# Kernel optimization log

Measured on AMD Instinct MI355X. Metric: run time of the kernel, lower is better.

Reference implementation:

```python
import jax, jax.numpy as jnp
import numpy as np

B, T, H = 4, 512, 512          # batch, num_target_nodes, hidden
V = 32000                       # static vocab
S, SDV = 512, 300               # source nodes, source dynamic vocab
TDV = 512                       # target dynamic vocab


def setup_inputs() -> dict:
    key = jax.random.key(0)
    ks = jax.random.split(key, 9)
    src_idx = jax.random.randint(ks[6], (B, S), 0, SDV)
    tgt_idx = jax.random.randint(ks[8], (B, T), 0, TDV)
    return {
        "hiddens": jax.random.normal(ks[0], (B, T, H), jnp.float32),
        "Wp": jax.random.normal(ks[1], (H, 3), jnp.float32) * (1.0 / np.sqrt(H)),
        "bp": jnp.zeros((3,), jnp.float32),
        "Wv": jax.random.normal(ks[2], (H, V), jnp.float32) * (1.0 / np.sqrt(H)),
        "bv": jnp.zeros((V,), jnp.float32),
        "source_attentions": jax.nn.softmax(jax.random.normal(ks[3], (B, T, S), jnp.float32), axis=-1),
        "source_attention_maps": jax.nn.one_hot(src_idx, SDV, dtype=jnp.float32),
        "target_attentions": jax.nn.softmax(jax.random.normal(ks[4], (B, T, TDV), jnp.float32), axis=-1),
        "target_attention_maps": jax.nn.one_hot(tgt_idx, TDV, dtype=jnp.float32),
    }


def reference(hiddens, Wp, bp, Wv, bv, source_attentions, source_attention_maps,
              target_attentions, target_attention_maps):
    b, t, h = hiddens.shape
    hf = hiddens.reshape(b * t, h)
    # switch probabilities: [copy_source, copy_target, generate]
    p = jax.nn.softmax(hf @ Wp + bp, axis=1).reshape(b, t, 3)
    p_copy_source = p[..., 0:1]
    p_copy_target = p[..., 1:2]
    p_generate = p[..., 2:3]
    # vocab scores with pad index masked to -inf (vocab_pad_idx = 0)
    scores = hf @ Wv + bv                      # [b*t, V]
    scores = scores.at[:, 0].set(-jnp.inf)
    vocab_probs = jax.nn.softmax(scores.reshape(b, t, -1), axis=-1)
    scaled_vocab_probs = vocab_probs * p_generate
    # copy distributions via one-hot scatter-sum (dense matmul in original)
    scaled_copy_source_probs = jnp.einsum(
        'bts,bsv->btv', source_attentions * p_copy_source, source_attention_maps)
    scaled_copy_target_probs = jnp.einsum(
        'btn,bnv->btv', target_attentions * p_copy_target, target_attention_maps)
    probs = jnp.concatenate(
        [scaled_vocab_probs, scaled_copy_source_probs, scaled_copy_target_probs], axis=2)
    predictions = jnp.argmax(probs, axis=2)
    return (probs, predictions)
```

## Files before the change

### kernel.cpp

```cpp
#include <hip/hip_runtime.h>
#include <hip/hip_bf16.h>
#include <math.h>

#define Bq   4
#define Tq   512
#define Hq   512
#define Vq   32000
#define Sq   512
#define SDVq 300
#define TDVq 512
#define ROWS (Bq * Tq)
#define OUTW (Vq + SDVq + TDVq)
#define NBLK (Vq / 128)

typedef __bf16 bf16x8 __attribute__((ext_vector_type(8)));
typedef float  fx4    __attribute__((ext_vector_type(4)));
typedef unsigned short ushort8 __attribute__((ext_vector_type(8)));

__device__ __forceinline__ void async16(const void* g, void* l) {
    __builtin_amdgcn_global_load_lds(
        (const __attribute__((address_space(1))) void*)g,
        (__attribute__((address_space(3))) void*)l, 16, 0, 0);
}

__device__ __forceinline__ float bf2f(unsigned short u) {
    union { unsigned int i; float f; } c;
    c.i = ((unsigned int)u) << 16;
    return c.f;
}

__global__ void compute_p(const float* __restrict__ hiddens,
                          const float* __restrict__ Wp,
                          const float* __restrict__ bp,
                          float* __restrict__ p) {
    int row  = blockIdx.x;
    int lane = threadIdx.x;
    const float* h = hiddens + (size_t)row * Hq;
    float a0 = 0.f, a1 = 0.f, a2 = 0.f;
    for (int i = lane; i < Hq; i += 64) {
        float hv = h[i];
        a0 += hv * Wp[i * 3 + 0];
        a1 += hv * Wp[i * 3 + 1];
        a2 += hv * Wp[i * 3 + 2];
    }
    for (int off = 32; off > 0; off >>= 1) {
        a0 += __shfl_down(a0, off);
        a1 += __shfl_down(a1, off);
        a2 += __shfl_down(a2, off);
    }
    if (lane == 0) {
        float l0 = a0 + bp[0], l1 = a1 + bp[1], l2 = a2 + bp[2];
        float M  = fmaxf(l0, fmaxf(l1, l2));
        float e0 = expf(l0 - M), e1 = expf(l1 - M), e2 = expf(l2 - M);
        float inv = 1.f / (e0 + e1 + e2);
        p[row * 3 + 0] = e0 * inv;
        p[row * 3 + 1] = e1 * inv;
        p[row * 3 + 2] = e2 * inv;
    }
}

__global__ void extract_idx(const float* __restrict__ map, int ncols,
                            int* __restrict__ idx) {
    int row  = blockIdx.x;
    int lane = threadIdx.x;
    const float* r = map + (size_t)row * ncols;
    float best = -1.f; int bi = 0;
    for (int i = lane; i < ncols; i += 64) {
        float v = r[i];
        if (v > best) { best = v; bi = i; }
    }
    for (int off = 32; off > 0; off >>= 1) {
        float ob  = __shfl_down(best, off);
        int   obi = __shfl_down(bi, off);
        if (ob > best) { best = ob; bi = obi; }
    }
    if (lane == 0) idx[row] = bi;
}

__global__ __launch_bounds__(256)
void convert_a(const float* __restrict__ in, __hip_bfloat16* __restrict__ o) {
    int i = blockIdx.x * 256 + threadIdx.x;
    float4 v = ((const float4*)in)[i];
    __hip_bfloat16* op = o + (size_t)i * 4;
    op[0] = __float2bfloat16(v.x);
    op[1] = __float2bfloat16(v.y);
    op[2] = __float2bfloat16(v.z);
    op[3] = __float2bfloat16(v.w);
}

__global__ __launch_bounds__(256)
void transpose_wv(const float* __restrict__ Wv, __hip_bfloat16* __restrict__ Wt) {
    __shared__ float t[32][33];
    int n0 = blockIdx.x * 32, k0 = blockIdx.y * 32;
    int tx = threadIdx.x, ty = threadIdx.y;
#pragma unroll
    for (int r = 0; r < 4; ++r)
        t[ty + r * 8][tx] = Wv[(size_t)(k0 + ty + r * 8) * Vq + n0 + tx];
    __syncthreads();
#pragma unroll
    for (int r = 0; r < 4; ++r)
        Wt[(size_t)(n0 + ty + r * 8) * Hq + k0 + tx] =
            __float2bfloat16(t[tx][ty + r * 8]);
}

__global__ __launch_bounds__(256)
void gemm_mfma(const __hip_bfloat16* __restrict__ A,
               const __hip_bfloat16* __restrict__ Bt,
               const float* __restrict__ bv,
               __hip_bfloat16* __restrict__ eb,
               float* __restrict__ partial) {
    __shared__ __align__(16) unsigned short As[3 * 4096];
    __shared__ __align__(16) unsigned short Bs[3 * 4096];
    __shared__ float rs[128];
    int tid  = threadIdx.x;
    int wave = tid >> 6, lane = tid & 63;

    int bid = blockIdx.x;
    int logical = (bid & 7) * 500 + (bid >> 3);
    int nb = logical >> 4;
    int mb = logical & 15;
    int bm = mb * 128;
    int bn = nb * 128;

    int wr = wave >> 1, wc = wave & 1;
    int lr = lane & 15;
    int kq = lane >> 4;

    fx4 acc[4][4];
#pragma unroll
    for (int i = 0; i < 4; ++i)
#pragma unroll
        for (int j = 0; j < 4; ++j)
            acc[i][j] = (fx4){0.f, 0.f, 0.f, 0.f};

    int c0 = tid, c1 = tid + 256;
    int ar0 = c0 & 127, ak0 = (c0 >> 7) * 8;
    int ar1 = c1 & 127, ak1 = (c1 >> 7) * 8;
    const unsigned short* Ag = (const unsigned short*)A;
    const unsigned short* Bg = (const unsigned short*)Bt;

#define STAGE(tt, bb) do {                                                   \
        int k0s = (tt) * 32;                                                 \
        unsigned short* Ab = &As[(bb) * 4096 + (wave << 6) * 8];             \
        unsigned short* Bb = &Bs[(bb) * 4096 + (wave << 6) * 8];             \
        async16(Ag + (size_t)(bm + ar0) * Hq + k0s + ak0, Ab);               \
        async16(Ag + (size_t)(bm + ar1) * Hq + k0s + ak1, Ab + 2048);        \
        async16(Bg + (size_t)(bn + ar0) * Hq + k0s + ak0, Bb);               \
        async16(Bg + (size_t)(bn + ar1) * Hq + k0s + ak1, Bb + 2048);        \
    } while (0)

    STAGE(0, 0);
    STAGE(1, 1);

#pragma unroll
    for (int t = 0; t < 16; ++t) {
        if (t < 15) asm volatile("s_waitcnt vmcnt(4)" ::: "memory");
        else        asm volatile("s_waitcnt vmcnt(0)" ::: "memory");
        __builtin_amdgcn_s_barrier();
        asm volatile("" ::: "memory");

        if (t + 2 < 16) STAGE(t + 2, (t + 2) % 3);

        const unsigned short* Asb = &As[(t % 3) * 4096];
        const unsigned short* Bsb = &Bs[(t % 3) * 4096];
        bf16x8 af[4], bfr[4];
#pragma unroll
        for (int i = 0; i < 4; ++i)
            af[i] = *(const bf16x8*)&Asb[(size_t)(kq * 128 + wr * 64 + i * 16 + lr) * 8];
#pragma unroll
        for (int j = 0; j < 4; ++j)
            bfr[j] = *(const bf16x8*)&Bsb[(size_t)(kq * 128 + wc * 64 + j * 16 + lr) * 8];

#pragma unroll
        for (int i = 0; i < 4; ++i)
#pragma unroll
            for (int j = 0; j < 4; ++j)
                acc[i][j] = __builtin_amdgcn_mfma_f32_16x16x32_bf16(
                    af[i], bfr[j], acc[i][j], 0, 0, 0);

        asm volatile("s_waitcnt lgkmcnt(0)" ::: "memory");
    }
#undef STAGE

    if (tid < 128) rs[tid] = 0.f;
    __syncthreads();

    float bvv[4];
#pragma unroll
    for (int j = 0; j < 4; ++j)
        bvv[j] = bv[bn + wc * 64 + j * 16 + lr];

#pragma unroll
    for (int i = 0; i < 4; ++i) {
        int lrow = wr * 64 + i * 16 + kq * 4;
        float rsum[4] = {0.f, 0.f, 0.f, 0.f};
#pragma unroll
        for (int j = 0; j < 4; ++j) {
            int gc = bn + wc * 64 + j * 16 + lr;
#pragma unroll
            for (int r = 0; r < 4; ++r) {
                float v = __expf(acc[i][j][r] + bvv[j]);
                if (gc == 0) v = 0.f;
                eb[(size_t)(bm + lrow + r) * Vq + gc] = __float2bfloat16(v);
                rsum[r] += v;
            }
        }
#pragma unroll
        for (int off = 1; off < 16; off <<= 1) {
#pragma unroll
            for (int r = 0; r < 4; ++r)
                rsum[r] += __shfl_xor(rsum[r], off);
        }
        if (lr == 0) {
#pragma unroll
            for (int r = 0; r < 4; ++r)
                atomicAdd(&rs[lrow + r], rsum[r]);
        }
    }
    __syncthreads();
    if (tid < 128) partial[(size_t)nb * ROWS + bm + tid] = rs[tid];
}

__global__ __launch_bounds__(256)
void finalize(const __hip_bfloat16* __restrict__ e_bf,
              const float* __restrict__ partial,
              const float* __restrict__ p,
              const float* __restrict__ src_att, const int* __restrict__ sidx,
              const float* __restrict__ tgt_att, const int* __restrict__ tidx,
              float* __restrict__ out, float* __restrict__ pred) {
    int row = blockIdx.x;
    int tid = threadIdx.x;
    int b   = row >> 9;
    __shared__ float accs[TDVq];
    __shared__ float bs[256];
    __shared__ int   is_[256];
    __shared__ float sred[4];

    float s = 0.f;
    for (int nb = tid; nb < NBLK; nb += 256)
        s += partial[(size_t)nb * ROWS + row];
    for (int off = 32; off > 0; off >>= 1) s += __shfl_down(s, off);
    if ((tid & 63) == 0) sred[tid >> 6] = s;
    __syncthreads();
    float S     = sred[0] + sred[1] + sred[2] + sred[3];
    float scale = p[row * 3 + 2] / S;

    const ushort8* er = (const ushort8*)(e_bf + (size_t)row * Vq);
    float* orow = out + (size_t)row * OUTW;
    float4* ov  = (float4*)orow;
    float bm_ = -1.f; int bi = 0;
    for (int i = tid; i < Vq / 8; i += 256) {
        ushort8 v = er[i];
        float f[8];
#pragma unroll
        for (int k = 0; k < 8; ++k) f[k] = bf2f(v[k]);
#pragma unroll
        for (int k = 0; k < 8; ++k)
            if (f[k] > bm_) { bm_ = f[k]; bi = i * 8 + k; }
        float4 lo = {f[0] * scale, f[1] * scale, f[2] * scale, f[3] * scale};
        float4 hi = {f[4] * scale, f[5] * scale, f[6] * scale, f[7] * scale};
        ov[2 * i]     = lo;
        ov[2 * i + 1] = hi;
    }
    bs[tid] = bm_; is_[tid] = bi;
    __syncthreads();
    for (int st = 128; st > 0; st >>= 1) {
        if (tid < st) {
            float v2 = bs[tid + st]; int i2 = is_[tid + st];
            if (v2 > bs[tid] || (v2 == bs[tid] && i2 < is_[tid])) {
                bs[tid] = v2; is_[tid] = i2;
            }
        }
        __syncthreads();
    }
    float cv0 = bs[0] * scale; int ci0 = is_[0];
    __syncthreads();

    for (int i = tid; i < SDVq; i += 256) accs[i] = 0.f;
    __syncthreads();
    {
        const float* arow = src_att + (size_t)row * Sq;
        const int*   ib   = sidx + b * Sq;
        for (int s2 = tid; s2 < Sq; s2 += 256)
            atomicAdd(&accs[ib[s2]], arow[s2]);
    }
    __syncthreads();
    {
        float pc = p[row * 3 + 0];
        float bm2 = -INFINITY; int bi2 = 0;
        for (int v = tid; v < SDVq; v += 256) {
            float val = accs[v] * pc;
            orow[Vq + v] = val;
            if (val > bm2) { bm2 = val; bi2 = v; }
        }
        bs[tid] = bm2; is_[tid] = bi2;
    }
    __syncthreads();
    for (int st = 128; st > 0; st >>= 1) {
        if (tid < st) {
            float v2 = bs[tid + st]; int i2 = is_[tid + st];
            if (v2 > bs[tid] || (v2 == bs[tid] && i2 < is_[tid])) {
                bs[tid] = v2; is_[tid] = i2;
            }
        }
        __syncthreads();
    }
    float cv1 = bs[0]; int ci1 = Vq + is_[0];
    __syncthreads();

    for (int i = tid; i < TDVq; i += 256) accs[i] = 0.f;
    __syncthreads();
    {
        const float* arow = tgt_att + (size_t)row * TDVq;
        const int*   ib   = tidx + b * TDVq;
        for (int s2 = tid; s2 < TDVq; s2 += 256)
            atomicAdd(&accs[ib[s2]], arow[s2]);
    }
    __syncthreads();
    {
        float pc = p[row * 3 + 1];
        float bm2 = -INFINITY; int bi2 = 0;
        for (int v = tid; v < TDVq; v += 256) {
            float val = accs[v] * pc;
            orow[Vq + SDVq + v] = val;
            if (val > bm2) { bm2 = val; bi2 = v; }
        }
        bs[tid] = bm2; is_[tid] = bi2;
    }
    __syncthreads();
    for (int st = 128; st > 0; st >>= 1) {
        if (tid < st) {
            float v2 = bs[tid + st]; int i2 = is_[tid + st];
            if (v2 > bs[tid] || (v2 == bs[tid] && i2 < is_[tid])) {
                bs[tid] = v2; is_[tid] = i2;
            }
        }
        __syncthreads();
    }

    if (tid == 0) {
        float cv2 = bs[0]; int ci2 = Vq + SDVq + is_[0];
        float v = cv0; int i = ci0;
        if (cv1 > v) { v = cv1; i = ci1; }
        if (cv2 > v) { v = cv2; i = ci2; }
        pred[row] = (float)i;
    }
}

extern "C" void kernel_launch(void* const* d_in, const int* in_sizes, int n_in,
                              void* d_out, int out_size, void* d_ws, size_t ws_size,
                              hipStream_t stream) {
    const float* hiddens = (const float*)d_in[0];
    const float* Wp      = (const float*)d_in[1];
    const float* bp      = (const float*)d_in[2];
    const float* Wv      = (const float*)d_in[3];
    const float* bv      = (const float*)d_in[4];
    const float* src_att = (const float*)d_in[5];
    const float* src_map = (const float*)d_in[6];
    const float* tgt_att = (const float*)d_in[7];
    const float* tgt_map = (const float*)d_in[8];

    float* out  = (float*)d_out;
    float* pred = out + (size_t)ROWS * OUTW;

    char* ws = (char*)d_ws;
    float* p_ws    = (float*)(ws);
    int*   sidx    = (int*)(ws + (24 << 10));
    int*   tidx    = (int*)(ws + (32 << 10));
    float* partial = (float*)(ws + (64 << 10));
    __hip_bfloat16* A_bf = (__hip_bfloat16*)(ws + (64 << 10) + (2 << 20));
    __hip_bfloat16* e_bf = (__hip_bfloat16*)(ws + (64 << 10) + (4 << 20));
    __hip_bfloat16* Wt   = (__hip_bfloat16*)(ws + (64 << 10) + (4 << 20) + (128 << 20));

    convert_a<<<ROWS * Hq / 4 / 256, 256, 0, stream>>>(hiddens, A_bf);
    {
        dim3 tg(Vq / 32, Hq / 32);
        dim3 tb(32, 8);
        transpose_wv<<<tg, tb, 0, stream>>>(Wv, Wt);
    }

    compute_p<<<ROWS, 64, 0, stream>>>(hiddens, Wp, bp, p_ws);
    extract_idx<<<Bq * Sq, 64, 0, stream>>>(src_map, SDVq, sidx);
    extract_idx<<<Bq * Tq, 64, 0, stream>>>(tgt_map, TDVq, tidx);

    gemm_mfma<<<(ROWS / 128) * NBLK, 256, 0, stream>>>(A_bf, Wt, bv, e_bf, partial);

    finalize<<<ROWS, 256, 0, stream>>>(e_bf, partial, p_ws,
                                       src_att, sidx, tgt_att, tidx, out, pred);
}
```

Before: 570.2 us.

## Make vocab GEMM persistent with cross-tile prefetch and per-wave partial sums

Replaces the one-block-per-tile GEMM with a persistent kernel of 768 blocks, each walking a contiguous range of 128x128 tiles. The triple-buffered LDS pipeline now runs across tile boundaries, so the next tile's first k-slices load during the current tile's tail and epilogue. MFMA issue is wrapped in s_setprio. The LDS atomic row-sum reduction is replaced by direct per-wave partial writes in a row-major layout that finalize reads contiguously. The cost is more complex slot indexing and uneven tile counts per block.

Result: slower. 586.4 us (+2.9%).

```diff
diff --git a/kernel.cpp b/kernel.cpp
--- a/kernel.cpp
+++ b/kernel.cpp
@@ -11,7 +11,9 @@
 #define TDVq 512
 #define ROWS (Bq * Tq)
 #define OUTW (Vq + SDVq + TDVq)
-#define NBLK (Vq / 128)
+#define NUNITS 4000
+#define GBLK 768
+#define PCOLS 512
 
 typedef __bf16 bf16x8 __attribute__((ext_vector_type(8)));
 typedef float  fx4    __attribute__((ext_vector_type(4)));
@@ -28,6 +30,8 @@
     c.i = ((unsigned int)u) << 16;
     return c.f;
 }
+
+__device__ __forceinline__ int m3(int a) { return a >= 3 ? a - 3 : a; }
 
 __global__ void compute_p(const float* __restrict__ hiddens,
                           const float* __restrict__ Wp,
@@ -103,122 +107,136 @@
             __float2bfloat16(t[tx][ty + r * 8]);
 }
 
-__global__ __launch_bounds__(256)
-void gemm_mfma(const __hip_bfloat16* __restrict__ A,
-               const __hip_bfloat16* __restrict__ Bt,
-               const float* __restrict__ bv,
-               __hip_bfloat16* __restrict__ eb,
-               float* __restrict__ partial) {
+__global__ __launch_bounds__(256, 3)
+void gemm_persist(const __hip_bfloat16* __restrict__ A,
+                  const __hip_bfloat16* __restrict__ Bt,
+                  const float* __restrict__ bv,
+                  __hip_bfloat16* __restrict__ eb,
+                  float* __restrict__ partial) {
     __shared__ __align__(16) unsigned short As[3 * 4096];
     __shared__ __align__(16) unsigned short Bs[3 * 4096];
-    __shared__ float rs[128];
     int tid  = threadIdx.x;
     int wave = tid >> 6, lane = tid & 63;
-
-    int bid = blockIdx.x;
-    int logical = (bid & 7) * 500 + (bid >> 3);
-    int nb = logical >> 4;
-    int mb = logical & 15;
-    int bm = mb * 128;
-    int bn = nb * 128;
-
     int wr = wave >> 1, wc = wave & 1;
     int lr = lane & 15;
     int kq = lane >> 4;
 
-    fx4 acc[4][4];
-#pragma unroll
-    for (int i = 0; i < 4; ++i)
-#pragma unroll
-        for (int j = 0; j < 4; ++j)
-            acc[i][j] = (fx4){0.f, 0.f, 0.f, 0.f};
-
-    int c0 = tid, c1 = tid + 256;
-    int ar0 = c0 & 127, ak0 = (c0 >> 7) * 8;
-    int ar1 = c1 & 127, ak1 = (c1 >> 7) * 8;
+    int x = blockIdx.x & 7, sl0 = blockIdx.x >> 3;
+    int chunk = x * 96 + sl0;
+    int u0 = (chunk * 125) / 24;
+    int u1 = ((chunk + 1) * 125) / 24;
+
+    int ar0 = tid & 127, ak0 = (tid >> 7) * 8;
     const unsigned short* Ag = (const unsigned short*)A;
     const unsigned short* Bg = (const unsigned short*)Bt;
-
-#define STAGE(tt, bb) do {                                                   \
-        int k0s = (tt) * 32;                                                 \
-        unsigned short* Ab = &As[(bb) * 4096 + (wave << 6) * 8];             \
-        unsigned short* Bb = &Bs[(bb) * 4096 + (wave << 6) * 8];             \
-        async16(Ag + (size_t)(bm + ar0) * Hq + k0s + ak0, Ab);               \
-        async16(Ag + (size_t)(bm + ar1) * Hq + k0s + ak1, Ab + 2048);        \
-        async16(Bg + (size_t)(bn + ar0) * Hq + k0s + ak0, Bb);               \
-        async16(Bg + (size_t)(bn + ar1) * Hq + k0s + ak1, Bb + 2048);        \
+    unsigned short* Alds = &As[(wave << 6) * 8];
+    unsigned short* Blds = &Bs[(wave << 6) * 8];
+
+#define SRC_A(u) (Ag + (size_t)(((u) & 15) * 128 + ar0) * Hq + ak0)
+#define SRC_B(u) (Bg + (size_t)(((u) >> 4) * 128 + ar0) * Hq + ak0)
+#define STAGE(pa, pb, k0s, slot) do {                                   \
+        async16((pa) + (k0s),      Alds + (slot) * 4096);               \
+        async16((pa) + (k0s) + 16, Alds + (slot) * 4096 + 2048);        \
+        async16((pb) + (k0s),      Blds + (slot) * 4096);               \
+        async16((pb) + (k0s) + 16, Blds + (slot) * 4096 + 2048);        \
     } while (0)
 
-    STAGE(0, 0);
-    STAGE(1, 1);
-
-#pragma unroll
-    for (int t = 0; t < 16; ++t) {
-        if (t < 15) asm volatile("s_waitcnt vmcnt(4)" ::: "memory");
-        else        asm volatile("s_waitcnt vmcnt(0)" ::: "memory");
-        __builtin_amdgcn_s_barrier();
-        asm volatile("" ::: "memory");
-
-        if (t + 2 < 16) STAGE(t + 2, (t + 2) % 3);
-
-        const unsigned short* Asb = &As[(t % 3) * 4096];
-        const unsigned short* Bsb = &Bs[(t % 3) * 4096];
-        bf16x8 af[4], bfr[4];
+    const unsigned short* pA = SRC_A(u0);
+    const unsigned short* pB = SRC_B(u0);
+    STAGE(pA, pB, 0,  0);
+    STAGE(pA, pB, 32, 1);
+
+    int ph = 0;
+    for (int u = u0; u < u1; ++u) {
+        int nb = u >> 4;
+        int bm = (u & 15) * 128, bn = nb * 128;
+        bool hasN = (u + 1 < u1);
+        int un = hasN ? u + 1 : u;
+        const unsigned short* nA = SRC_A(un);
+        const unsigned short* nB = SRC_B(un);
+
+        float bvv[4];
+#pragma unroll
+        for (int j = 0; j < 4; ++j)
+            bvv[j] = bv[bn + wc * 64 + j * 16 + lr];
+
+        fx4 acc[4][4];
 #pragma unroll
         for (int i = 0; i < 4; ++i)
-            af[i] = *(const bf16x8*)&Asb[(size_t)(kq * 128 + wr * 64 + i * 16 + lr) * 8];
-#pragma unroll
-        for (int j = 0; j < 4; ++j)
-            bfr[j] = *(const bf16x8*)&Bsb[(size_t)(kq * 128 + wc * 64 + j * 16 + lr) * 8];
-
-#pragma unroll
-        for (int i = 0; i < 4; ++i)
 #pragma unroll
             for (int j = 0; j < 4; ++j)
-                acc[i][j] = __builtin_amdgcn_mfma_f32_16x16x32_bf16(
-                    af[i], bfr[j], acc[i][j], 0, 0, 0);
-
-        asm volatile("s_waitcnt lgkmcnt(0)" ::: "memory");
+                acc[i][j] = (fx4){0.f, 0.f, 0.f, 0.f};
+
+#pragma unroll
+        for (int tk = 0; tk < 16; ++tk) {
+            if (tk == 15 && !hasN)
+                asm volatile("s_waitcnt vmcnt(0)" ::: "memory");
+            else
+                asm volatile("s_waitcnt vmcnt(4)" ::: "memory");
+            __builtin_amdgcn_s_barrier();
+            asm volatile("" ::: "memory");
+
+            if (tk < 14)
+                STAGE(pA, pB, (tk + 2) * 32, m3(ph + (tk + 2) % 3));
+            else if (hasN)
+                STAGE(nA, nB, (tk - 14) * 32, m3(ph + (tk + 2) % 3));
+
+            int sl = m3(ph + tk % 3);
+            const unsigned short* Asb = &As[sl * 4096];
+            const unsigned short* Bsb = &Bs[sl * 4096];
+            bf16x8 af[4], bfr[4];
+#pragma unroll
+            for (int i = 0; i < 4; ++i)
+                af[i] = *(const bf16x8*)&Asb[(size_t)(kq * 128 + wr * 64 + i * 16 + lr) * 8];
+#pragma unroll
+            for (int j = 0; j < 4; ++j)
+                bfr[j] = *(const bf16x8*)&Bsb[(size_t)(kq * 128 + wc * 64 + j * 16 + lr) * 8];
+
+            __builtin_amdgcn_s_setprio(1);
+#pragma unroll
+            for (int i = 0; i < 4; ++i)
+#pragma unroll
+                for (int j = 0; j < 4; ++j)
+                    acc[i][j] = __builtin_amdgcn_mfma_f32_16x16x32_bf16(
+                        af[i], bfr[j], acc[i][j], 0, 0, 0);
+            __builtin_amdgcn_s_setprio(0);
+
+            asm volatile("s_waitcnt lgkmcnt(0)" ::: "memory");
+        }
+
+#pragma unroll
+        for (int i = 0; i < 4; ++i) {
+            int lrow = wr * 64 + i * 16 + kq * 4;
+            float rsum[4] = {0.f, 0.f, 0.f, 0.f};
+#pragma unroll
+            for (int j = 0; j < 4; ++j) {
+                int gc = bn + wc * 64 + j * 16 + lr;
+#pragma unroll
+                for (int r = 0; r < 4; ++r) {
+                    float v = __expf(acc[i][j][r] + bvv[j]);
+                    if (gc == 0) v = 0.f;
+                    eb[(size_t)(bm + lrow + r) * Vq + gc] = __float2bfloat16(v);
+                    rsum[r] += v;
+                }
+            }
+#pragma unroll
+            for (int off = 1; off < 16; off <<= 1)
+#pragma unroll
+                for (int r = 0; r < 4; ++r)
+                    rsum[r] += __shfl_xor(rsum[r], off);
+            if (lr == 0) {
+#pragma unroll
+                for (int r = 0; r < 4; ++r)
+                    partial[(size_t)(bm + lrow + r) * PCOLS + nb * 2 + wc] = rsum[r];
+            }
+        }
+
+        pA = nA; pB = nB;
+        ph = m3(ph + 1);
     }
 #undef STAGE
-
-    if (tid < 128) rs[tid] = 0.f;
-    __syncthreads();
-
-    float bvv[4];
-#pragma unroll
-    for (int j = 0; j < 4; ++j)
-        bvv[j] = bv[bn + wc * 64 + j * 16 + lr];
-
-#pragma unroll
-    for (int i = 0; i < 4; ++i) {
-        int lrow = wr * 64 + i * 16 + kq * 4;
-        float rsum[4] = {0.f, 0.f, 0.f, 0.f};
-#pragma unroll
-        for (int j = 0; j < 4; ++j) {
-            int gc = bn + wc * 64 + j * 16 + lr;
-#pragma unroll
-            for (int r = 0; r < 4; ++r) {
-                float v = __expf(acc[i][j][r] + bvv[j]);
-                if (gc == 0) v = 0.f;
-                eb[(size_t)(bm + lrow + r) * Vq + gc] = __float2bfloat16(v);
-                rsum[r] += v;
-            }
-        }
-#pragma unroll
-        for (int off = 1; off < 16; off <<= 1) {
-#pragma unroll
-            for (int r = 0; r < 4; ++r)
-                rsum[r] += __shfl_xor(rsum[r], off);
-        }
-        if (lr == 0) {
-#pragma unroll
-            for (int r = 0; r < 4; ++r)
-                atomicAdd(&rs[lrow + r], rsum[r]);
-        }
-    }
-    __syncthreads();
-    if (tid < 128) partial[(size_t)nb * ROWS + bm + tid] = rs[tid];
+#undef SRC_A
+#undef SRC_B
 }
 
 __global__ __launch_bounds__(256)
@@ -237,8 +255,8 @@
     __shared__ float sred[4];
 
     float s = 0.f;
-    for (int nb = tid; nb < NBLK; nb += 256)
-        s += partial[(size_t)nb * ROWS + row];
+    const float* prow = partial + (size_t)row * PCOLS;
+    for (int k = tid; k < 500; k += 256) s += prow[k];
     for (int off = 32; off > 0; off >>= 1) s += __shfl_down(s, off);
     if ((tid & 63) == 0) sred[tid >> 6] = s;
     __syncthreads();
@@ -368,9 +386,9 @@
     int*   sidx    = (int*)(ws + (24 << 10));
     int*   tidx    = (int*)(ws + (32 << 10));
     float* partial = (float*)(ws + (64 << 10));
-    __hip_bfloat16* A_bf = (__hip_bfloat16*)(ws + (64 << 10) + (2 << 20));
-    __hip_bfloat16* e_bf = (__hip_bfloat16*)(ws + (64 << 10) + (4 << 20));
-    __hip_bfloat16* Wt   = (__hip_bfloat16*)(ws + (64 << 10) + (4 << 20) + (128 << 20));
+    __hip_bfloat16* A_bf = (__hip_bfloat16*)(ws + (8 << 20));
+    __hip_bfloat16* e_bf = (__hip_bfloat16*)(ws + (12 << 20));
+    __hip_bfloat16* Wt   = (__hip_bfloat16*)(ws + (144 << 20));
 
     convert_a<<<ROWS * Hq / 4 / 256, 256, 0, stream>>>(hiddens, A_bf);
     {
@@ -383,7 +401,7 @@
     extract_idx<<<Bq * Sq, 64, 0, stream>>>(src_map, SDVq, sidx);
     extract_idx<<<Bq * Tq, 64, 0, stream>>>(tgt_map, TDVq, tidx);
 
-    gemm_mfma<<<(ROWS / 128) * NBLK, 256, 0, stream>>>(A_bf, Wt, bv, e_bf, partial);
+    gemm_persist<<<GBLK, 256, 0, stream>>>(A_bf, Wt, bv, e_bf, partial);
 
     finalize<<<ROWS, 256, 0, stream>>>(e_bf, partial, p_ws,
                                        src_att, sidx, tgt_att, tidx, out, pred);
```
